# Kernel tuning notes

Hardware: AMD Instinct MI355X
Metric: run time of the kernel (lower is better)

## Reference

```python
import jax, jax.numpy as jnp
import numpy as np

B, L, D, H = 4, 2048, 1024, 16
DK = D // H  # 64


def setup_inputs() -> dict:
    key = jax.random.key(0)
    ks = jax.random.split(key, 5)
    scale = 1.0 / np.sqrt(D)
    return {
        "x": jax.random.normal(ks[0], (B, L, D), dtype=jnp.float32),
        "Wq": jax.random.normal(ks[1], (D, D), dtype=jnp.float32) * scale,
        "Wk": jax.random.normal(ks[2], (D, D), dtype=jnp.float32) * scale,
        "Wv": jax.random.normal(ks[3], (D, D), dtype=jnp.float32) * scale,
        "Wo": jax.random.normal(ks[4], (D, D), dtype=jnp.float32) * scale,
    }


def reference(x, Wq, Wk, Wv, Wo):
    b, l, d = x.shape
    # Linear: y = x @ W^T (weight stored as [out, in], no bias)
    def proj(W):
        y = jnp.einsum('bld,ed->ble', x, W)            # [B,L,D]
        return y.reshape(b, l, H, DK).transpose(0, 2, 1, 3)  # [B,H,L,dk]
    Q, K, V = proj(Wq), proj(Wk), proj(Wv)
    scores = jnp.einsum('bhqd,bhkd->bhqk', Q, K) / jnp.sqrt(jnp.float32(DK))
    causal = jnp.tril(jnp.ones((l, l), dtype=bool))
    scores = jnp.where(causal[None, None, :, :], scores, jnp.float32(-1e30))
    attn = jax.nn.softmax(scores, axis=-1)             # stable softmax
    out = jnp.einsum('bhqk,bhkd->bhqd', attn, V)       # [B,H,L,dk]
    out = out.transpose(0, 2, 1, 3).reshape(b, l, d)   # [B,L,D]
    return jnp.einsum('bld,ed->ble', out, Wo)
```

## Files before the change

kernel.cpp:

```cpp
#include <hip/hip_runtime.h>
#include <hip/hip_bf16.h>
#include <stdint.h>

typedef short bf16x8 __attribute__((ext_vector_type(8)));
typedef float f32x4 __attribute__((ext_vector_type(4)));
typedef float f32x16 __attribute__((ext_vector_type(16)));
typedef unsigned int uint4v __attribute__((ext_vector_type(4)));

#define NB 4
#define NL 2048
#define ND 1024
#define NH 16
#define NDK 64
#define NM (NB*NL)
#define QSCALE 0.18033688011112042f

__device__ __forceinline__ ushort f2bf(float f) {
  __bf16 h = (__bf16)f;
  return __builtin_bit_cast(unsigned short, h);
}

__device__ __forceinline__ unsigned int cvtpk(float lo, float hi) {
  unsigned int d;
  asm("v_cvt_pk_bf16_f32 %0, %1, %2" : "=v"(d) : "v"(lo), "v"(hi));
  return d;
}

__device__ __forceinline__ void gload16(const void* g, void* l) {
  __builtin_amdgcn_global_load_lds(
      (__attribute__((address_space(1))) void*)(uintptr_t)g,
      (__attribute__((address_space(3))) void*)(uint32_t)(uintptr_t)l,
      16, 0, 0);
}

__device__ __forceinline__ f32x16 mfma32(bf16x8 a, bf16x8 b, f32x16 c) {
  return __builtin_amdgcn_mfma_f32_32x32x16_bf16(a, b, c, 0, 0, 0);
}
__device__ __forceinline__ f32x4 mfma16(bf16x8 a, bf16x8 b, f32x4 c) {
  return __builtin_amdgcn_mfma_f32_16x16x32_bf16(a, b, c, 0, 0, 0);
}

__global__ void convert_all(const float* __restrict__ x, const float* __restrict__ wq,
                            const float* __restrict__ wk, const float* __restrict__ wv,
                            const float* __restrict__ wo, ushort* __restrict__ o) {
  long i = (long)blockIdx.x * 256 + threadIdx.x;
  const long NX = 2097152;
  const long NW = 262144;
  const float4* s;
  long off;
  if (i < NX) { s = (const float4*)x; off = i; }
  else {
    long j = i - NX;
    int wsel = (int)(j >> 18);
    off = j & (NW - 1);
    s = (const float4*)(wsel == 0 ? wq : wsel == 1 ? wk : wsel == 2 ? wv : wo);
  }
  float4 v = s[off];
  ushort4 r;
  r.x = f2bf(v.x); r.y = f2bf(v.y); r.z = f2bf(v.z); r.w = f2bf(v.w);
  ((ushort4*)o)[i] = r;
}

template<int MODE>
__global__ __launch_bounds__(256, 4)
void gemm_bt(const ushort* __restrict__ A,
             const ushort* __restrict__ Bq, const ushort* __restrict__ Bk, const ushort* __restrict__ Bv,
             ushort* __restrict__ Oq, ushort* __restrict__ Ok, ushort* __restrict__ Ov,
             float* __restrict__ OF) {
  __shared__ __align__(16) ushort lA[2][128 * 32];
  __shared__ __align__(16) ushort lB[2][128 * 32];
  const int t = threadIdx.x;
  const int w = t >> 6, l = t & 63;
  const int lr = l & 15, lh = l >> 4;
  const int bxr = blockIdx.x;
  const int bx = (bxr & 7) * 8 + (bxr >> 3);
  const int m0 = bx * 128;
  const int ng = blockIdx.y * 128;
  const ushort* Bp;
  ushort* Op = nullptr;
  int mi = 0, n0;
  if (MODE == 0) {
    mi = ng >> 10;
    Bp = (mi == 0) ? Bq : (mi == 1) ? Bk : Bv;
    Op = (mi == 0) ? Oq : (mi == 1) ? Ok : Ov;
    n0 = ng & 1023;
  } else {
    Bp = Bq;
    n0 = ng;
  }
  const int wrow = (w >> 1) * 64, wcol = (w & 1) * 64;
  const int r = t >> 2, c = t & 3;
  const ushort* gA0 = A + (size_t)(m0 + r) * ND + c * 8;
  const ushort* gA1 = A + (size_t)(m0 + 64 + r) * ND + c * 8;
  const ushort* gB0 = Bp + (size_t)(n0 + r) * ND + c * 8;
  const ushort* gB1 = Bp + (size_t)(n0 + 64 + r) * ND + c * 8;

#define GSTAGE(bi, kofs) do {                              \
    gload16(gA0 + (kofs), &lA[bi][w * 512]);               \
    gload16(gA1 + (kofs), &lA[bi][2048 + w * 512]);        \
    gload16(gB0 + (kofs), &lB[bi][w * 512]);               \
    gload16(gB1 + (kofs), &lB[bi][2048 + w * 512]);        \
  } while (0)

  GSTAGE(0, 0);
  f32x4 acc[4][4] = {};
  for (int kt = 0; kt < ND; kt += 32) {
    const int buf = (kt >> 5) & 1;
    __syncthreads();
    if (kt + 32 < ND) GSTAGE(buf ^ 1, kt + 32);
    bf16x8 af[4], bfr[4];
#pragma unroll
    for (int mt = 0; mt < 4; mt++)
      af[mt] = *(const bf16x8*)&lA[buf][(wrow + mt * 16 + lr) * 32 + lh * 8];
#pragma unroll
    for (int nt = 0; nt < 4; nt++)
      bfr[nt] = *(const bf16x8*)&lB[buf][(wcol + nt * 16 + lr) * 32 + lh * 8];
#pragma unroll
    for (int mt = 0; mt < 4; mt++)
#pragma unroll
      for (int nt = 0; nt < 4; nt++)
        acc[mt][nt] = mfma16(af[mt], bfr[nt], acc[mt][nt]);
  }
#undef GSTAGE
#pragma unroll
  for (int mt = 0; mt < 4; mt++) {
#pragma unroll
    for (int nt = 0; nt < 4; nt++) {
      if (MODE == 0 && mi == 2) {
        int m = m0 + wrow + mt * 16 + lh * 4;
        int nl = n0 + wcol + nt * 16 + lr;
        int b = m >> 11, ll = m & 2047;
        int h = nl >> 6, dk = nl & 63;
        ushort4 vs;
        vs.x = f2bf(acc[mt][nt][0]); vs.y = f2bf(acc[mt][nt][1]);
        vs.z = f2bf(acc[mt][nt][2]); vs.w = f2bf(acc[mt][nt][3]);
        *(ushort4*)&Op[(((size_t)(b * NH + h)) * NDK + dk) * NL + ll] = vs;
      } else {
#pragma unroll
        for (int j = 0; j < 4; j++) {
          int m = m0 + wrow + mt * 16 + lh * 4 + j;
          int n = wcol + nt * 16 + lr;
          if (MODE == 0) {
            int nl = n0 + n;
            int b = m >> 11, ll = m & 2047;
            int h = nl >> 6, dk = nl & 63;
            float v = acc[mt][nt][j];
            if (mi == 0) v *= QSCALE;
            Op[(((size_t)(b * NH + h)) * NL + ll) * NDK + dk] = f2bf(v);
          } else {
            OF[(size_t)m * ND + ng + n] = acc[mt][nt][j];
          }
        }
      }
    }
  }
}

__global__ __launch_bounds__(256, 3)
void attn_fwd(const ushort* __restrict__ Q, const ushort* __restrict__ Kg,
              const ushort* __restrict__ VT, ushort* __restrict__ O) {
  __shared__ __align__(16) ushort lK[3][64 * 64];
  __shared__ __align__(16) ushort lV[3][64 * 64];
  const int t = threadIdx.x;
  const int w = t >> 6, l = t & 63;
  const int l31 = l & 31, hi = l >> 5;
  const int id = blockIdx.x;
  const int bh = id & 63;
  const int qt = 15 - (id >> 6);
  const size_t base = (size_t)bh * (NL * NDK);
  const int q0w = qt * 128 + w * 32;
  const int ktmax = q0w >> 6;
  const int NT = qt * 2 + 2;

  bf16x8 qf[4];
  {
    const ushort* qp = Q + base + (size_t)(q0w + l31) * NDK + hi * 8;
#pragma unroll
    for (int sl = 0; sl < 4; sl++) qf[sl] = *(const bf16x8*)(qp + sl * 16);
  }
  bf16x8 ones;
#pragma unroll
  for (int r = 0; r < 8; r++) ones[r] = (short)0x3F80;

  const int kr0 = t >> 3, kc0 = (t & 7) ^ (kr0 & 7);
  const int s1i = t + 256;
  const int kr1 = s1i >> 3, kc1 = (s1i & 7) ^ (kr1 & 7);
  const ushort* gK0 = Kg + base + (size_t)kr0 * NDK + kc0 * 8;
  const ushort* gK1 = Kg + base + (size_t)kr1 * NDK + kc1 * 8;
  const ushort* gV0 = VT + base + (size_t)kr0 * NL + kc0 * 8;
  const ushort* gV1 = VT + base + (size_t)kr1 * NL + kc1 * 8;

  f32x16 accO0 = {}, accO1 = {}, accS = {};
  const int swz = l31 & 7;

#define PACKPAIR(sv, plo, phi) do {                                          \
    unsigned int a0 = cvtpk(sv[0], sv[1]),   a1 = cvtpk(sv[2], sv[3]);       \
    unsigned int b0 = cvtpk(sv[4], sv[5]),   b1 = cvtpk(sv[6], sv[7]);       \
    unsigned int c0 = cvtpk(sv[8], sv[9]),   c1 = cvtpk(sv[10], sv[11]);     \
    unsigned int d0 = cvtpk(sv[12], sv[13]), d1 = cvtpk(sv[14], sv[15]);     \
    asm("v_permlane32_swap_b32 %0, %1" : "+v"(a0), "+v"(b0));                \
    asm("v_permlane32_swap_b32 %0, %1" : "+v"(a1), "+v"(b1));                \
    asm("v_permlane32_swap_b32 %0, %1" : "+v"(c0), "+v"(d0));                \
    asm("v_permlane32_swap_b32 %0, %1" : "+v"(c1), "+v"(d1));                \
    uint4v lo_; lo_[0] = a0; lo_[1] = a1; lo_[2] = b0; lo_[3] = b1;          \
    uint4v hi_; hi_[0] = c0; hi_[1] = c1; hi_[2] = d0; hi_[3] = d1;          \
    plo = __builtin_bit_cast(bf16x8, lo_);                                   \
    phi = __builtin_bit_cast(bf16x8, hi_);                                   \
  } while (0)

#define STAGE(slot, kt1) do {                                       \
    const size_t kvn = (size_t)(kt1) * 64;                          \
    gload16(gK0 + kvn * NDK, &lK[slot][w * 512]);                   \
    gload16(gK1 + kvn * NDK, &lK[slot][2048 + w * 512]);            \
    gload16(gV0 + kvn, &lV[slot][w * 512]);                         \
    gload16(gV1 + kvn, &lV[slot][2048 + w * 512]);                  \
  } while (0)

  STAGE(0, 0);
  STAGE(1, 1);

  int scur = 0, snxt = 2;
  for (int kt = 0; kt < NT; kt++) {
    if (kt + 1 < NT) asm volatile("s_waitcnt vmcnt(4)" ::: "memory");
    else             asm volatile("s_waitcnt vmcnt(0)" ::: "memory");
    __builtin_amdgcn_s_barrier();
    __builtin_amdgcn_sched_barrier(0);
    if (kt + 2 < NT) STAGE(snxt, kt + 2);
    if (kt <= ktmax) {
      const ushort* bK = lK[scur];
      const ushort* bV = lV[scur];
      const bool dtile = (kt == ktmax);
      const bool skipHi = dtile && !(w & 1);
      f32x16 s0 = {}, s1v = {};
      __builtin_amdgcn_s_setprio(1);
#pragma unroll
      for (int sl = 0; sl < 4; sl++) {
        int c = 2 * sl + hi;
        bf16x8 kf0 = *(const bf16x8*)&bK[l31 * 64 + ((c ^ swz) * 8)];
        s0 = mfma32(kf0, qf[sl], s0);
      }
      if (!skipHi) {
#pragma unroll
        for (int sl = 0; sl < 4; sl++) {
          int c = 2 * sl + hi;
          bf16x8 kf1 = *(const bf16x8*)&bK[(32 + l31) * 64 + ((c ^ swz) * 8)];
          s1v = mfma32(kf1, qf[sl], s1v);
        }
      }
      __builtin_amdgcn_s_setprio(0);
      if (dtile) {
        if (!(w & 1)) {
#pragma unroll
          for (int r = 0; r < 16; r++) {
            int kvo = (r & 3) + 8 * (r >> 2) + 4 * hi;
            if (kvo > l31) s0[r] = -1e30f;
          }
        } else {
#pragma unroll
          for (int r = 0; r < 16; r++) {
            int kvo = (r & 3) + 8 * (r >> 2) + 4 * hi;
            if (kvo > l31) s1v[r] = -1e30f;
          }
        }
      }
#pragma unroll
      for (int r = 0; r < 16; r++) s0[r] = exp2f(s0[r]);
      if (!skipHi) {
#pragma unroll
        for (int r = 0; r < 16; r++) s1v[r] = exp2f(s1v[r]);
      }
      bf16x8 pa[4];
      PACKPAIR(s0, pa[0], pa[1]);
      if (!skipHi) PACKPAIR(s1v, pa[2], pa[3]);
      __builtin_amdgcn_s_setprio(1);
#pragma unroll
      for (int ks = 0; ks < 2; ks++) {
        int c = 2 * ks + hi;
        bf16x8 vf0 = *(const bf16x8*)&bV[l31 * 64 + ((c ^ swz) * 8)];
        bf16x8 vf1 = *(const bf16x8*)&bV[(32 + l31) * 64 + ((c ^ swz) * 8)];
        accO0 = mfma32(vf0, pa[ks], accO0);
        accO1 = mfma32(vf1, pa[ks], accO1);
        accS = mfma32(ones, pa[ks], accS);
      }
      if (!skipHi) {
#pragma unroll
        for (int ks = 2; ks < 4; ks++) {
          int c = 2 * ks + hi;
          bf16x8 vf0 = *(const bf16x8*)&bV[l31 * 64 + ((c ^ swz) * 8)];
          bf16x8 vf1 = *(const bf16x8*)&bV[(32 + l31) * 64 + ((c ^ swz) * 8)];
          accO0 = mfma32(vf0, pa[ks], accO0);
          accO1 = mfma32(vf1, pa[ks], accO1);
          accS = mfma32(ones, pa[ks], accS);
        }
      }
      __builtin_amdgcn_s_setprio(0);
    }
    scur = (scur + 1 == 3) ? 0 : scur + 1;
    snxt = (snxt + 1 == 3) ? 0 : snxt + 1;
  }
#undef STAGE
#undef PACKPAIR
  const int b = bh >> 4, h = bh & 15;
  const float inv = 1.0f / accS[0];
  const int q = q0w + l31;
  ushort* orow = O + ((size_t)b * NL + q) * ND + h * NDK;
#pragma unroll
  for (int gi = 0; gi < 4; gi++) {
    ushort4 o0, o1;
    o0.x = f2bf(accO0[4 * gi + 0] * inv); o0.y = f2bf(accO0[4 * gi + 1] * inv);
    o0.z = f2bf(accO0[4 * gi + 2] * inv); o0.w = f2bf(accO0[4 * gi + 3] * inv);
    o1.x = f2bf(accO1[4 * gi + 0] * inv); o1.y = f2bf(accO1[4 * gi + 1] * inv);
    o1.z = f2bf(accO1[4 * gi + 2] * inv); o1.w = f2bf(accO1[4 * gi + 3] * inv);
    *(ushort4*)&orow[8 * gi + 4 * hi] = o0;
    *(ushort4*)&orow[32 + 8 * gi + 4 * hi] = o1;
  }
}

extern "C" void kernel_launch(void* const* d_in, const int* in_sizes, int n_in,
                              void* d_out, int out_size, void* d_ws, size_t ws_size,
                              hipStream_t stream) {
  const float* x = (const float*)d_in[0];
  const float* wq = (const float*)d_in[1];
  const float* wk = (const float*)d_in[2];
  const float* wv = (const float*)d_in[3];
  const float* wo = (const float*)d_in[4];
  char* ws = (char*)d_ws;
  ushort* xb  = (ushort*)(ws);
  ushort* wqb = (ushort*)(ws + 16777216);
  ushort* wkb = (ushort*)(ws + 18874368);
  ushort* wvb = (ushort*)(ws + 20971520);
  ushort* wob = (ushort*)(ws + 23068672);
  ushort* Qb  = (ushort*)(ws + 25165824);
  ushort* Kb  = (ushort*)(ws + 41943040);
  ushort* Vb  = (ushort*)(ws + 58720256);
  ushort* Ob  = (ushort*)(ws + 75497472);

  convert_all<<<12288, 256, 0, stream>>>(x, wq, wk, wv, wo, xb);
  gemm_bt<0><<<dim3(64, 24), 256, 0, stream>>>(xb, wqb, wkb, wvb, Qb, Kb, Vb, nullptr);
  attn_fwd<<<dim3(1024), 256, 0, stream>>>(Qb, Kb, Vb, Ob);
  gemm_bt<1><<<dim3(64, 8), 256, 0, stream>>>(Ob, wob, nullptr, nullptr,
                                              nullptr, nullptr, nullptr, (float*)d_out);
}
```

Baseline: 155.9 us.

## Fuse fp32-to-bf16 conversion of x into the QKV projection GEMM

Drops the separate conversion pass over the activation tensor x. The QKV GEMM now loads fp32 x tiles straight into LDS with an XOR swizzle and converts them to bf16 with packed converts while building MFMA fragments. This removes one full write and re-read of x in bf16, but doubles the LDS footprint and global bytes for the A operand. It also lowers the occupancy hint from 4 to 3 blocks per CU, and every block that shares an A tile now repeats the conversion. The output GEMM is split into its own kernel with unchanged logic.

```diff
diff --git a/kernel.cpp b/kernel.cpp
--- a/kernel.cpp
+++ b/kernel.cpp
@@ -40,34 +40,25 @@
   return __builtin_amdgcn_mfma_f32_16x16x32_bf16(a, b, c, 0, 0, 0);
 }
 
-__global__ void convert_all(const float* __restrict__ x, const float* __restrict__ wq,
-                            const float* __restrict__ wk, const float* __restrict__ wv,
-                            const float* __restrict__ wo, ushort* __restrict__ o) {
+__global__ void convert_w(const float* __restrict__ wq, const float* __restrict__ wk,
+                          const float* __restrict__ wv, const float* __restrict__ wo,
+                          ushort* __restrict__ o) {
   long i = (long)blockIdx.x * 256 + threadIdx.x;
-  const long NX = 2097152;
   const long NW = 262144;
-  const float4* s;
-  long off;
-  if (i < NX) { s = (const float4*)x; off = i; }
-  else {
-    long j = i - NX;
-    int wsel = (int)(j >> 18);
-    off = j & (NW - 1);
-    s = (const float4*)(wsel == 0 ? wq : wsel == 1 ? wk : wsel == 2 ? wv : wo);
-  }
+  int wsel = (int)(i >> 18);
+  long off = i & (NW - 1);
+  const float4* s = (const float4*)(wsel == 0 ? wq : wsel == 1 ? wk : wsel == 2 ? wv : wo);
   float4 v = s[off];
   ushort4 r;
   r.x = f2bf(v.x); r.y = f2bf(v.y); r.z = f2bf(v.z); r.w = f2bf(v.w);
   ((ushort4*)o)[i] = r;
 }
 
-template<int MODE>
-__global__ __launch_bounds__(256, 4)
-void gemm_bt(const ushort* __restrict__ A,
-             const ushort* __restrict__ Bq, const ushort* __restrict__ Bk, const ushort* __restrict__ Bv,
-             ushort* __restrict__ Oq, ushort* __restrict__ Ok, ushort* __restrict__ Ov,
-             float* __restrict__ OF) {
-  __shared__ __align__(16) ushort lA[2][128 * 32];
+__global__ __launch_bounds__(256, 3)
+void gemm_qkv(const float* __restrict__ X,
+              const ushort* __restrict__ Bq, const ushort* __restrict__ Bk, const ushort* __restrict__ Bv,
+              ushort* __restrict__ Oq, ushort* __restrict__ Ok, ushort* __restrict__ Ov) {
+  __shared__ __align__(16) float  lA[2][128 * 32];
   __shared__ __align__(16) ushort lB[2][128 * 32];
   const int t = threadIdx.x;
   const int w = t >> 6, l = t & 63;
@@ -76,42 +67,45 @@
   const int bx = (bxr & 7) * 8 + (bxr >> 3);
   const int m0 = bx * 128;
   const int ng = blockIdx.y * 128;
-  const ushort* Bp;
-  ushort* Op = nullptr;
-  int mi = 0, n0;
-  if (MODE == 0) {
-    mi = ng >> 10;
-    Bp = (mi == 0) ? Bq : (mi == 1) ? Bk : Bv;
-    Op = (mi == 0) ? Oq : (mi == 1) ? Ok : Ov;
-    n0 = ng & 1023;
-  } else {
-    Bp = Bq;
-    n0 = ng;
-  }
+  const int mi = ng >> 10;
+  const int n0 = ng & 1023;
+  const ushort* Bp = (mi == 0) ? Bq : (mi == 1) ? Bk : Bv;
+  ushort* Op = (mi == 0) ? Oq : (mi == 1) ? Ok : Ov;
   const int wrow = (w >> 1) * 64, wcol = (w & 1) * 64;
-  const int r = t >> 2, c = t & 3;
-  const ushort* gA0 = A + (size_t)(m0 + r) * ND + c * 8;
-  const ushort* gA1 = A + (size_t)(m0 + 64 + r) * ND + c * 8;
-  const ushort* gB0 = Bp + (size_t)(n0 + r) * ND + c * 8;
-  const ushort* gB1 = Bp + (size_t)(n0 + 64 + r) * ND + c * 8;
-
-#define GSTAGE(bi, kofs) do {                              \
-    gload16(gA0 + (kofs), &lA[bi][w * 512]);               \
-    gload16(gA1 + (kofs), &lA[bi][2048 + w * 512]);        \
-    gload16(gB0 + (kofs), &lB[bi][w * 512]);               \
-    gload16(gB1 + (kofs), &lB[bi][2048 + w * 512]);        \
+  const int rB = t >> 2, cB = t & 3;
+  const ushort* gB0 = Bp + (size_t)(n0 + rB) * ND + cB * 8;
+  const ushort* gB1 = Bp + (size_t)(n0 + 64 + rB) * ND + cB * 8;
+  const int rA = t >> 3;
+  const int cSw = (t & 7) ^ (rA & 7);
+  const float* gA = X + (size_t)(m0 + rA) * ND + cSw * 4;
+
+#define QSTAGE(bi, kofs) do {                                            \
+    gload16(gA + (size_t)0  * ND + (kofs), &lA[bi][0    + w * 256]);     \
+    gload16(gA + (size_t)32 * ND + (kofs), &lA[bi][1024 + w * 256]);     \
+    gload16(gA + (size_t)64 * ND + (kofs), &lA[bi][2048 + w * 256]);     \
+    gload16(gA + (size_t)96 * ND + (kofs), &lA[bi][3072 + w * 256]);     \
+    gload16(gB0 + (kofs), &lB[bi][w * 512]);                             \
+    gload16(gB1 + (kofs), &lB[bi][2048 + w * 512]);                      \
   } while (0)
 
-  GSTAGE(0, 0);
+  QSTAGE(0, 0);
   f32x4 acc[4][4] = {};
+  const int swzA = lr & 7;
   for (int kt = 0; kt < ND; kt += 32) {
     const int buf = (kt >> 5) & 1;
     __syncthreads();
-    if (kt + 32 < ND) GSTAGE(buf ^ 1, kt + 32);
+    if (kt + 32 < ND) QSTAGE(buf ^ 1, kt + 32);
     bf16x8 af[4], bfr[4];
 #pragma unroll
-    for (int mt = 0; mt < 4; mt++)
-      af[mt] = *(const bf16x8*)&lA[buf][(wrow + mt * 16 + lr) * 32 + lh * 8];
+    for (int mt = 0; mt < 4; mt++) {
+      const int R = wrow + mt * 16 + lr;
+      const float4 fa = *(const float4*)&lA[buf][R * 32 + (((2 * lh) ^ swzA) * 4)];
+      const float4 fb = *(const float4*)&lA[buf][R * 32 + (((2 * lh + 1) ^ swzA) * 4)];
+      uint4v u;
+      u[0] = cvtpk(fa.x, fa.y); u[1] = cvtpk(fa.z, fa.w);
+      u[2] = cvtpk(fb.x, fb.y); u[3] = cvtpk(fb.z, fb.w);
+      af[mt] = __builtin_bit_cast(bf16x8, u);
+    }
 #pragma unroll
     for (int nt = 0; nt < 4; nt++)
       bfr[nt] = *(const bf16x8*)&lB[buf][(wcol + nt * 16 + lr) * 32 + lh * 8];
@@ -121,12 +115,12 @@
       for (int nt = 0; nt < 4; nt++)
         acc[mt][nt] = mfma16(af[mt], bfr[nt], acc[mt][nt]);
   }
-#undef GSTAGE
+#undef QSTAGE
 #pragma unroll
   for (int mt = 0; mt < 4; mt++) {
 #pragma unroll
     for (int nt = 0; nt < 4; nt++) {
-      if (MODE == 0 && mi == 2) {
+      if (mi == 2) {
         int m = m0 + wrow + mt * 16 + lh * 4;
         int nl = n0 + wcol + nt * 16 + lr;
         int b = m >> 11, ll = m & 2047;
@@ -139,21 +133,74 @@
 #pragma unroll
         for (int j = 0; j < 4; j++) {
           int m = m0 + wrow + mt * 16 + lh * 4 + j;
-          int n = wcol + nt * 16 + lr;
-          if (MODE == 0) {
-            int nl = n0 + n;
-            int b = m >> 11, ll = m & 2047;
-            int h = nl >> 6, dk = nl & 63;
-            float v = acc[mt][nt][j];
-            if (mi == 0) v *= QSCALE;
-            Op[(((size_t)(b * NH + h)) * NL + ll) * NDK + dk] = f2bf(v);
-          } else {
-            OF[(size_t)m * ND + ng + n] = acc[mt][nt][j];
-          }
+          int nl = n0 + wcol + nt * 16 + lr;
+          int b = m >> 11, ll = m & 2047;
+          int h = nl >> 6, dk = nl & 63;
+          float v = acc[mt][nt][j];
+          if (mi == 0) v *= QSCALE;
+          Op[(((size_t)(b * NH + h)) * NL + ll) * NDK + dk] = f2bf(v);
         }
       }
     }
   }
+}
+
+__global__ __launch_bounds__(256, 4)
+void gemm_out(const ushort* __restrict__ A, const ushort* __restrict__ Bw,
+              float* __restrict__ OF) {
+  __shared__ __align__(16) ushort lA[2][128 * 32];
+  __shared__ __align__(16) ushort lB[2][128 * 32];
+  const int t = threadIdx.x;
+  const int w = t >> 6, l = t & 63;
+  const int lr = l & 15, lh = l >> 4;
+  const int bxr = blockIdx.x;
+  const int bx = (bxr & 7) * 8 + (bxr >> 3);
+  const int m0 = bx * 128;
+  const int n0 = blockIdx.y * 128;
+  const int wrow = (w >> 1) * 64, wcol = (w & 1) * 64;
+  const int r = t >> 2, c = t & 3;
+  const ushort* gA0 = A + (size_t)(m0 + r) * ND + c * 8;
+  const ushort* gA1 = A + (size_t)(m0 + 64 + r) * ND + c * 8;
+  const ushort* gB0 = Bw + (size_t)(n0 + r) * ND + c * 8;
+  const ushort* gB1 = Bw + (size_t)(n0 + 64 + r) * ND + c * 8;
+
+#define GSTAGE(bi, kofs) do {                              \
+    gload16(gA0 + (kofs), &lA[bi][w * 512]);               \
+    gload16(gA1 + (kofs), &lA[bi][2048 + w * 512]);        \
+    gload16(gB0 + (kofs), &lB[bi][w * 512]);               \
+    gload16(gB1 + (kofs), &lB[bi][2048 + w * 512]);        \
+  } while (0)
+
+  GSTAGE(0, 0);
+  f32x4 acc[4][4] = {};
+  for (int kt = 0; kt < ND; kt += 32) {
+    const int buf = (kt >> 5) & 1;
+    __syncthreads();
+    if (kt + 32 < ND) GSTAGE(buf ^ 1, kt + 32);
+    bf16x8 af[4], bfr[4];
+#pragma unroll
+    for (int mt = 0; mt < 4; mt++)
+      af[mt] = *(const bf16x8*)&lA[buf][(wrow + mt * 16 + lr) * 32 + lh * 8];
+#pragma unroll
+    for (int nt = 0; nt < 4; nt++)
+      bfr[nt] = *(const bf16x8*)&lB[buf][(wcol + nt * 16 + lr) * 32 + lh * 8];
+#pragma unroll
+    for (int mt = 0; mt < 4; mt++)
+#pragma unroll
+      for (int nt = 0; nt < 4; nt++)
+        acc[mt][nt] = mfma16(af[mt], bfr[nt], acc[mt][nt]);
+  }
+#undef GSTAGE
+#pragma unroll
+  for (int mt = 0; mt < 4; mt++)
+#pragma unroll
+    for (int nt = 0; nt < 4; nt++)
+#pragma unroll
+      for (int j = 0; j < 4; j++) {
+        int m = m0 + wrow + mt * 16 + lh * 4 + j;
+        int n = wcol + nt * 16 + lr;
+        OF[(size_t)m * ND + n0 + n] = acc[mt][nt][j];
+      }
 }
 
 __global__ __launch_bounds__(256, 3)
@@ -325,19 +372,17 @@
   const float* wv = (const float*)d_in[3];
   const float* wo = (const float*)d_in[4];
   char* ws = (char*)d_ws;
-  ushort* xb  = (ushort*)(ws);
   ushort* wqb = (ushort*)(ws + 16777216);
-  ushort* wkb = (ushort*)(ws + 18874368);
-  ushort* wvb = (ushort*)(ws + 20971520);
   ushort* wob = (ushort*)(ws + 23068672);
   ushort* Qb  = (ushort*)(ws + 25165824);
   ushort* Kb  = (ushort*)(ws + 41943040);
   ushort* Vb  = (ushort*)(ws + 58720256);
   ushort* Ob  = (ushort*)(ws + 75497472);
-
-  convert_all<<<12288, 256, 0, stream>>>(x, wq, wk, wv, wo, xb);
-  gemm_bt<0><<<dim3(64, 24), 256, 0, stream>>>(xb, wqb, wkb, wvb, Qb, Kb, Vb, nullptr);
+  ushort* wkb = (ushort*)(ws + 18874368);
+  ushort* wvb = (ushort*)(ws + 20971520);
+
+  convert_w<<<4096, 256, 0, stream>>>(wq, wk, wv, wo, wqb);
+  gemm_qkv<<<dim3(64, 24), 256, 0, stream>>>(x, wqb, wkb, wvb, Qb, Kb, Vb);
   attn_fwd<<<dim3(1024), 256, 0, stream>>>(Qb, Kb, Vb, Ob);
-  gemm_bt<1><<<dim3(64, 8), 256, 0, stream>>>(Ob, wob, nullptr, nullptr,
-                                              nullptr, nullptr, nullptr, (float*)d_out);
-}
+  gemm_out<<<dim3(64, 8), 256, 0, stream>>>(Ob, wob, (float*)d_out);
+}
```

New measurement: 161.5 us. 3.6% more time.
